# Kernel optimization log

Hardware: AMD Instinct MI355X
Metric: run time of the kernel (lower is better)

The kernel has to match this reference:

```python
import jax, jax.numpy as jnp
import numpy as np

B, CIN, HID, HEADS, K, STRIDE, PAD, W = 8, 256, 256, 8, 31, 1, 15, 16384
HD = HID // HEADS  # head dim
DN = ('NCHW', 'OIHW', 'NCHW')


def setup_inputs() -> dict:
    key = jax.random.key(0)
    ks = jax.random.split(key, 6)
    std = 1.0 / np.sqrt(HD)
    return dict(
        x=jax.random.normal(ks[0], (B, CIN, 1, W), jnp.float32),
        query=(jax.random.normal(ks[1], (HID,), jnp.float32) * std),
        Wk=(jax.random.normal(ks[2], (CIN, HID), jnp.float32) * std),
        Wk_bias=jnp.zeros((HID,), jnp.float32),
        rpe=0.02 * jax.random.normal(ks[3], (HEADS, 1, 1, K), jnp.float32),
        to_v_w=(jax.random.normal(ks[4], (HID, CIN, 1, 1), jnp.float32) / np.sqrt(CIN)),
        to_v_b=jnp.zeros((HID,), jnp.float32),
        to_out_w=(jax.random.normal(ks[5], (HID, HID, 1, 1), jnp.float32) / np.sqrt(HID)),
        to_out_b=jnp.zeros((HID,), jnp.float32),
    )


def reference(x, query, Wk, Wk_bias, rpe, to_v_w, to_v_b, to_out_w, to_out_b):
    Bsz = x.shape[0]
    # shared learned query -> [B, heads, hd], normalized and scaled
    q = jnp.broadcast_to(query, (Bsz, HID)).reshape(Bsz, HEADS, HD)
    q = q / (jnp.linalg.norm(q, axis=-1, keepdims=True) + 1e-6)
    q = q / np.sqrt(HD)
    # fused QK: (q @ Wk^T) @ x  -> cost [B, heads, 1, W]
    Wk_r = Wk.reshape(CIN, HEADS, HD)
    qWk = jnp.einsum('bhd,Dhd->bDh', q, Wk_r)          # [B, CIN, heads]
    cost = jnp.einsum('bDhw,bDc->bchw', x, qWk)        # [B, heads, 1, W]
    qWk_b = jnp.einsum('hd,bhd->bh', Wk_bias.reshape(HEADS, HD), q)
    cost = cost + qWk_b[:, :, None, None]
    cost_exp = jnp.exp(cost)
    # v = 1x1 conv (to_v)
    v = jnp.einsum('bdhw,od->bohw', x, to_v_w.reshape(HID, CIN)) + to_v_b[None, :, None, None]
    # exp-weighted values, grouped windowed sums
    vc = (cost_exp[:, :, None] * v.reshape(Bsz, HEADS, HD, 1, W)).reshape(Bsz, HID, 1, W)
    rpe_exp = jnp.exp(rpe)                             # [heads, 1, 1, K]
    kern_v = jnp.repeat(rpe_exp, HD, axis=0)           # [HID, 1, 1, K] depthwise
    sum_v = jax.lax.conv_general_dilated(
        vc, kern_v, (1, STRIDE), ((0, 0), (PAD, PAD)),
        feature_group_count=HID, dimension_numbers=DN)
    sum_c = jax.lax.conv_general_dilated(
        cost_exp, rpe_exp, (1, STRIDE), ((0, 0), (PAD, PAD)),
        feature_group_count=HEADS, dimension_numbers=DN)
    Wo = sum_v.shape[-1]
    out = sum_v.reshape(Bsz, HEADS, HD, 1, Wo) / sum_c.reshape(Bsz, HEADS, 1, 1, Wo)
    out = out.reshape(Bsz, HID, 1, Wo)
    # to_out 1x1 conv
    out = jnp.einsum('bdhw,od->bohw', out, to_out_w.reshape(HID, HID)) + to_out_b[None, :, None, None]
    return out
```

## Files before the change

### kernel.cpp

```cpp
#include <hip/hip_runtime.h>
#include <hip/hip_bf16.h>
#include <math.h>

#define BATCH  8
#define NHEADS 8
#define KW     31
#define W      16384

#define WS_QWKB 2048
#define WS_RPE  2056
#define OFF_WVH 9216
#define OFF_WOH (OFF_WVH + 131072)
#define OFF_CE  (OFF_WOH + 131072)

typedef __attribute__((ext_vector_type(8))) short  short8;
typedef __attribute__((ext_vector_type(4))) float  f32x4;

__device__ __forceinline__ float f4c(const float4& v, int i) {
  switch (i) { case 0: return v.x; case 1: return v.y; case 2: return v.z; default: return v.w; }
}
__device__ __forceinline__ unsigned short f2bf(float f) {
  union { __hip_bfloat16 h; unsigned short u; } cv; cv.h = __float2bfloat16(f); return cv.u;
}
__device__ __forceinline__ float bf2f(unsigned short u) {
  union { __hip_bfloat16 h; unsigned short u; } cv; cv.u = u; return __bfloat162float(cv.h);
}

__global__ __launch_bounds__(256) void prep_kernel(
    const float* __restrict__ query, const float* __restrict__ Wk,
    const float* __restrict__ Wkb, const float* __restrict__ rpe,
    const float* __restrict__ Wv, const float* __restrict__ Wo,
    float* __restrict__ ws, unsigned short* __restrict__ WvH,
    unsigned short* __restrict__ WoH) {
  int t = threadIdx.x, bid = blockIdx.x;
  if (bid == 0) {
    __shared__ float q_l[256];
    float qv = query[t];
    float ss = qv * qv;
    #pragma unroll
    for (int m = 16; m >= 1; m >>= 1) ss += __shfl_xor(ss, m, 32);
    qv = qv / (sqrtf(ss) + 1e-6f) * 0.17677669529663687f;
    q_l[t] = qv;
    __syncthreads();
    const float* wr = Wk + (size_t)t * 256;
    #pragma unroll
    for (int h = 0; h < 8; ++h) {
      float s = 0.f;
      #pragma unroll
      for (int d = 0; d < 32; ++d) s = fmaf(q_l[h*32 + d], wr[h*32 + d], s);
      ws[t*8 + h] = s;
    }
    float pb = Wkb[t] * q_l[t];
    #pragma unroll
    for (int m = 16; m >= 1; m >>= 1) pb += __shfl_xor(pb, m, 32);
    if ((t & 31) == 0) ws[WS_QWKB + (t >> 5)] = pb;
    if (t < NHEADS * KW) ws[WS_RPE + t] = __expf(rpe[t]);
  } else {
    const float* src = (bid <= 4) ? Wv : Wo;
    unsigned short* dst = (bid <= 4) ? WvH : WoH;
    int seg = (bid - 1) & 3;
    int base4 = seg * 4096;
    #pragma unroll
    for (int it = 0; it < 16; ++it) {
      int i4 = base4 + t + 256 * it;
      float4 v = ((const float4*)src)[i4];
      ushort4 o;
      o.x = f2bf(v.x); o.y = f2bf(v.y); o.z = f2bf(v.z); o.w = f2bf(v.w);
      ((ushort4*)dst)[i4] = o;
    }
  }
}

__global__ __launch_bounds__(256, 2) void xv_kernel(
    const float* __restrict__ x, const float* __restrict__ wsf,
    const unsigned short* __restrict__ A,
    const float* __restrict__ bias,
    float* __restrict__ ceout, float* __restrict__ vcout, int b0) {
  __shared__ float xs[64 * 260];
  __shared__ float cbuf[2048];
  __shared__ float ceL[512];
  __shared__ float biasL[256];

  int t = threadIdx.x;
  int bb = blockIdx.y, b = b0 + bb;
  int w0 = blockIdx.x * 64;
  biasL[t] = bias[t];

  {
    int rr = t >> 4, c2 = t & 15;
    #pragma unroll
    for (int db = 0; db < 4; ++db) {
      float4 v0 = *(const float4*)(x + ((size_t)b*256 + db*64 + rr*4 + 0)*W + w0 + c2*4);
      float4 v1 = *(const float4*)(x + ((size_t)b*256 + db*64 + rr*4 + 1)*W + w0 + c2*4);
      float4 v2 = *(const float4*)(x + ((size_t)b*256 + db*64 + rr*4 + 2)*W + w0 + c2*4);
      float4 v3 = *(const float4*)(x + ((size_t)b*256 + db*64 + rr*4 + 3)*W + w0 + c2*4);
      #pragma unroll
      for (int i = 0; i < 4; ++i) {
        float4 tv = make_float4(f4c(v0,i), f4c(v1,i), f4c(v2,i), f4c(v3,i));
        *(float4*)&xs[(c2*4 + i)*260 + db*64 + rr*4] = tv;
      }
    }
  }
  __syncthreads();

  int w = t & 63, q = t >> 6;
  int qu = __builtin_amdgcn_readfirstlane(q);

  f32x4 xr[16];
  {
    const float* xrow = &xs[w*260 + qu*64];
    #pragma unroll
    for (int i = 0; i < 16; ++i) xr[i] = *(const f32x4*)(xrow + 4*i);
    float ca[8] = {0,0,0,0,0,0,0,0};
    const float* qkb = wsf + (size_t)qu*64*8;
    #pragma unroll
    for (int k8 = 0; k8 < 8; ++k8) {
      const float* qr = qkb + 64*k8;
      #pragma unroll
      for (int e = 0; e < 4; ++e) {
        #pragma unroll
        for (int h = 0; h < 8; ++h) {
          ca[h] = fmaf(xr[2*k8][e],   qr[e*8 + h],     ca[h]);
          ca[h] = fmaf(xr[2*k8+1][e], qr[(e+4)*8 + h], ca[h]);
        }
      }
    }
    #pragma unroll
    for (int h = 0; h < 8; ++h) cbuf[t*8 + h] = ca[h];
  }
  __syncthreads();

  {
    unsigned short* hrow = (unsigned short*)xs + w*520 + qu*64;
    #pragma unroll
    for (int k8 = 0; k8 < 8; ++k8) {
      short8 hs, ls;
      #pragma unroll
      for (int e = 0; e < 4; ++e) {
        float a0 = xr[2*k8][e], a1 = xr[2*k8+1][e];
        unsigned short h0 = f2bf(a0), h1 = f2bf(a1);
        hs[e]   = (short)h0;  hs[e+4] = (short)h1;
        ls[e]   = (short)f2bf(a0 - bf2f(h0));
        ls[e+4] = (short)f2bf(a1 - bf2f(h1));
      }
      *(short8*)(hrow + 8*k8)       = hs;
      *(short8*)(hrow + 256 + 8*k8) = ls;
    }
  }
  __syncthreads();

  #pragma unroll
  for (int s = 0; s < 2; ++s) {
    int idx = t + 256*s;
    int h = idx >> 6, ww = idx & 63;
    float sum = cbuf[ww*8 + h] + cbuf[(64+ww)*8 + h] + cbuf[(128+ww)*8 + h]
              + cbuf[(192+ww)*8 + h] + wsf[WS_QWKB + h];
    float ce = __expf(sum);
    ceL[h*64 + ww] = ce;
    ceout[((size_t)bb*8 + h)*W + w0 + ww] = ce;
  }
  __syncthreads();

  int wid = t >> 6, quad = (t >> 4) & 3, m = t & 15;
  f32x4 acc[4][4];
  #pragma unroll
  for (int j = 0; j < 4; ++j)
    #pragma unroll
    for (int c = 0; c < 4; ++c) acc[j][c] = (f32x4){0.f, 0.f, 0.f, 0.f};

  const unsigned short* xsu = (const unsigned short*)xs;
  #pragma unroll
  for (int kk = 0; kk < 8; ++kk) {
    int ko = kk*32 + quad*8;
    short8 a[4], bh[4], bl[4];
    #pragma unroll
    for (int j = 0; j < 4; ++j)
      a[j] = *(const short8*)(A + (size_t)(64*wid + 16*j + m)*256 + ko);
    #pragma unroll
    for (int c = 0; c < 4; ++c) {
      int rw = 16*c + m;
      bh[c] = *(const short8*)(xsu + rw*520 + ko);
      bl[c] = *(const short8*)(xsu + rw*520 + 256 + ko);
    }
    #pragma unroll
    for (int j = 0; j < 4; ++j)
      #pragma unroll
      for (int c = 0; c < 4; ++c) {
        acc[j][c] = __builtin_amdgcn_mfma_f32_16x16x32_bf16(a[j], bh[c], acc[j][c], 0, 0, 0);
        acc[j][c] = __builtin_amdgcn_mfma_f32_16x16x32_bf16(a[j], bl[c], acc[j][c], 0, 0, 0);
      }
  }
  __syncthreads();

  #pragma unroll
  for (int j = 0; j < 4; ++j) {
    int ob = 64*wid + 16*j + 4*quad;
    int h = (64*wid + 16*j) >> 5;
    #pragma unroll
    for (int c = 0; c < 4; ++c) {
      int wc = 16*c + m;
      float ce = ceL[h*64 + wc];
      f32x4 r;
      #pragma unroll
      for (int i = 0; i < 4; ++i) r[i] = (acc[j][c][i] + biasL[ob + i]) * ce;
      *(f32x4*)(xs + wc*260 + ob) = r;
    }
  }
  __syncthreads();
  {
    size_t rowbase = (size_t)bb*W + w0;
    int w2 = t >> 2;
    #pragma unroll
    for (int k = 0; k < 16; ++k) {
      int oq = (t & 3)*64 + 4*k;
      f32x4 v = *(const f32x4*)(xs + w2*260 + oq);
      *(f32x4*)(vcout + (rowbase + w2)*256 + oq) = v;
    }
  }
}

template<int MODE>
__global__ __launch_bounds__(256, 2) void gemm_kernel(
    const unsigned short* __restrict__ A, const float* __restrict__ bias,
    const float* __restrict__ cost, unsigned short* Bact,
    float* outp, int b0) {
  __shared__ float smem[17408];
  __shared__ float ceL[512];
  __shared__ float biasL[256];
  unsigned short* smem_u = (unsigned short*)smem;

  int t = threadIdx.x;
  int bb = blockIdx.y;
  int w0 = blockIdx.x * 64;

  biasL[t] = bias[t];
  if (MODE == 0) {
    #pragma unroll
    for (int s = 0; s < 2; ++s) {
      int i = t + 256*s;
      ceL[i] = cost[((size_t)(bb*8 + (i >> 6)))*W + w0 + (i & 63)];
    }
  }
  {
    const unsigned short* src = Bact + ((size_t)bb*W + w0)*512;
    #pragma unroll
    for (int it = 0; it < 16; ++it) {
      int idx = t + 256*it;
      int r = idx >> 5, col = (idx & 31) * 8;
      short8 v = *(const short8*)(src + (size_t)idx*8);
      *(short8*)(smem_u + r*264 + col) = v;
    }
  }
  __syncthreads();

  int wid = t >> 6, quad = (t >> 4) & 3, m = t & 15;
  f32x4 acc[4][4];
  #pragma unroll
  for (int j = 0; j < 4; ++j)
    #pragma unroll
    for (int c = 0; c < 4; ++c) acc[j][c] = (f32x4){0.f, 0.f, 0.f, 0.f};

  #pragma unroll
  for (int kk = 0; kk < 8; ++kk) {
    int ko = kk*32 + quad*8;
    short8 a[4], bh[4], bl[4];
    #pragma unroll
    for (int j = 0; j < 4; ++j)
      a[j] = *(const short8*)(A + (size_t)(64*wid + 16*j + m)*256 + ko);
    #pragma unroll
    for (int c = 0; c < 4; ++c) {
      int row = 2*(16*c + m);
      bh[c] = *(const short8*)(smem_u + row*264 + ko);
      bl[c] = *(const short8*)(smem_u + (row+1)*264 + ko);
    }
    #pragma unroll
    for (int j = 0; j < 4; ++j)
      #pragma unroll
      for (int c = 0; c < 4; ++c) {
        acc[j][c] = __builtin_amdgcn_mfma_f32_16x16x32_bf16(a[j], bh[c], acc[j][c], 0, 0, 0);
        acc[j][c] = __builtin_amdgcn_mfma_f32_16x16x32_bf16(a[j], bl[c], acc[j][c], 0, 0, 0);
      }
  }
  __syncthreads();

  if (MODE == 0) {
    #pragma unroll
    for (int j = 0; j < 4; ++j) {
      int ob = 64*wid + 16*j + 4*quad;
      int h = (64*wid + 16*j) >> 5;
      #pragma unroll
      for (int c = 0; c < 4; ++c) {
        int w = 16*c + m;
        float ce = ceL[h*64 + w];
        f32x4 r;
        #pragma unroll
        for (int i = 0; i < 4; ++i) r[i] = (acc[j][c][i] + biasL[ob + i]) * ce;
        *(f32x4*)(smem + w*260 + ob) = r;
      }
    }
    __syncthreads();
    float* vcg = (float*)Bact;
    size_t rowbase = (size_t)bb*W + w0;
    int w = t >> 2;
    #pragma unroll
    for (int k = 0; k < 16; ++k) {
      int oq = (t & 3)*64 + 4*k;
      f32x4 v = *(const f32x4*)(smem + w*260 + oq);
      *(f32x4*)(vcg + (rowbase + w)*256 + oq) = v;
    }
  } else {
    #pragma unroll
    for (int j = 0; j < 4; ++j) {
      int ob = 64*wid + 16*j + 4*quad;
      #pragma unroll
      for (int c = 0; c < 4; ++c) {
        int w = 16*c + m;
        #pragma unroll
        for (int i = 0; i < 4; ++i) smem[(ob + i)*68 + w] = acc[j][c][i] + biasL[ob + i];
      }
    }
    __syncthreads();
    float* og = outp + (size_t)(b0 + bb)*256*W;
    #pragma unroll
    for (int i = 0; i < 4; ++i) {
      int o = (t >> 2) + 64*i;
      int c4 = t & 3;
      #pragma unroll
      for (int k = 0; k < 4; ++k) {
        int w = (c4 + 4*k)*4;
        f32x4 v = *(const f32x4*)(smem + o*68 + w);
        *(f32x4*)(og + (size_t)o*W + w0 + w) = v;
      }
    }
  }
}

__global__ __launch_bounds__(256, 2) void conv_kernel(
    const float* __restrict__ vc, const float* __restrict__ costexp,
    const float* __restrict__ rpe_ws, unsigned short* __restrict__ u) {
  __shared__ float vcl[94 * 132];
  __shared__ float cel[8 * 96];
  __shared__ float rcl[8 * 64];
  __shared__ float rpel[8 * 32];

  int t = threadIdx.x;
  int half = blockIdx.y, bb = blockIdx.z;
  int w0 = blockIdx.x * 64;

  rpel[t] = ((t & 31) < KW) ? rpe_ws[(t >> 5)*KW + (t & 31)] : 0.f;
  #pragma unroll
  for (int it = 0; it < 3; ++it) {
    int idx = t + 256*it;
    int h = idx / 96, c = idx % 96;
    if (h < 8) {
      int gw = w0 - 15 + c;
      cel[idx] = (c < 94 && gw >= 0 && gw < W) ? costexp[((size_t)bb*8 + h)*W + gw] : 0.f;
    }
  }
  #pragma unroll
  for (int it = 0; it < 12; ++it) {
    int idx = t + 256*it;
    int r = idx >> 5, c4 = (idx & 31)*4;
    if (r < 94) {
      int gw = w0 - 15 + r;
      float4 v = make_float4(0.f, 0.f, 0.f, 0.f);
      if (gw >= 0 && gw < W)
        v = *(const float4*)(vc + ((size_t)bb*W + gw)*256 + half*128 + c4);
      *(float4*)&vcl[r*132 + c4] = v;
    }
  }
  __syncthreads();

  #pragma unroll
  for (int s = 0; s < 2; ++s) {
    int idx = t + 256*s;
    int h = idx >> 6, w = idx & 63;
    float acc = 0.f;
    #pragma unroll
    for (int k = 0; k < KW; ++k) acc = fmaf(rpel[h*32 + k], cel[h*96 + w + k], acc);
    rcl[h*64 + w] = 1.0f / acc;
  }
  __syncthreads();

  int p = t & 63, g = t >> 6;
  int hh = half*4 + (p >> 4);
  float rp[KW];
  #pragma unroll
  for (int k = 0; k < KW; ++k) rp[k] = rpel[hh*32 + k];

  float ax[16], ay[16];
  #pragma unroll
  for (int i = 0; i < 16; ++i) { ax[i] = 0.f; ay[i] = 0.f; }
  #pragma unroll
  for (int s = 0; s < 46; ++s) {
    float2 v = *(const float2*)&vcl[(16*g + s)*132 + 2*p];
    #pragma unroll
    for (int i = 0; i < 16; ++i) {
      int k = s - i;
      if (k >= 0 && k < KW) {
        ax[i] = fmaf(rp[k], v.x, ax[i]);
        ay[i] = fmaf(rp[k], v.y, ay[i]);
      }
    }
  }
  #pragma unroll
  for (int i = 0; i < 16; ++i) {
    float rc = rcl[hh*64 + 16*g + i];
    float ux = ax[i] * rc, uy = ay[i] * rc;
    unsigned short hx = f2bf(ux), hy = f2bf(uy);
    unsigned short lx = f2bf(ux - bf2f(hx)), ly = f2bf(uy - bf2f(hy));
    unsigned short* ud = u + ((size_t)bb*W + w0 + 16*g + i)*512 + half*128 + 2*p;
    ushort2 hvv; hvv.x = hx; hvv.y = hy;
    ushort2 lvv; lvv.x = lx; lvv.y = ly;
    *(ushort2*)(ud)       = hvv;
    *(ushort2*)(ud + 256) = lvv;
  }
}

extern "C" void kernel_launch(void* const* d_in, const int* in_sizes, int n_in,
                              void* d_out, int out_size, void* d_ws, size_t ws_size,
                              hipStream_t stream) {
  const float* x     = (const float*)d_in[0];
  const float* query = (const float*)d_in[1];
  const float* Wk    = (const float*)d_in[2];
  const float* Wkb   = (const float*)d_in[3];
  const float* rpe   = (const float*)d_in[4];
  const float* Wv    = (const float*)d_in[5];
  const float* tvb   = (const float*)d_in[6];
  const float* Wo    = (const float*)d_in[7];
  const float* tob   = (const float*)d_in[8];
  float* out = (float*)d_out;
  char* wsb  = (char*)d_ws;
  float* wsf = (float*)d_ws;

  unsigned short* WvH = (unsigned short*)(wsb + OFF_WVH);
  unsigned short* WoH = (unsigned short*)(wsb + OFF_WOH);

  const size_t per_b = (size_t)8*W*4 + (size_t)W*256*4 + (size_t)W*512*2;
  int NB = (int)((ws_size > OFF_CE) ? ((ws_size - OFF_CE) / per_b) : 1);
  if (NB > BATCH) NB = BATCH;
  if (NB < 1) NB = 1;

  float*          ceB = (float*)(wsb + OFF_CE);
  float*          vcB = (float*)(wsb + OFF_CE + (size_t)NB*8*W*4);
  unsigned short* uB  = (unsigned short*)(wsb + OFF_CE + (size_t)NB*8*W*4 + (size_t)NB*W*256*4);

  prep_kernel<<<9, 256, 0, stream>>>(query, Wk, Wkb, rpe, Wv, Wo, wsf, WvH, WoH);

  for (int b0 = 0; b0 < BATCH; b0 += NB) {
    int nb = (BATCH - b0 < NB) ? (BATCH - b0) : NB;
    xv_kernel<<<dim3(256, nb), 256, 0, stream>>>(x, wsf, WvH, tvb, ceB, vcB, b0);
    conv_kernel<<<dim3(256, 2, nb), 256, 0, stream>>>(vcB, ceB, wsf + WS_RPE, uB);
    gemm_kernel<1><<<dim3(256, nb), 256, 0, stream>>>(WoH, tob, nullptr, uB, out, b0);
  }
}
```

Measured before the change: 470.0 us.

## Split work across more threads and blocks in xv, conv and out-GEMM kernels

xv_kernel moves to 512 threads per block, so each wave computes a 32-row slice of the value GEMM and half the K-reduction for the cost, with a two-phase cbuf reduction. conv_kernel splits channels into four quarters per block, which halves shared memory and per-thread accumulators. The output GEMM becomes a dedicated kernel that streams the hi and lo bf16 halves through a smaller LDS tile in two passes and writes results directly. The goal is higher occupancy and lower register and LDS pressure, at the cost of extra barriers, more redundant halo loads in conv, and uncoalesced strided output stores.

```diff
diff --git a/kernel.cpp b/kernel.cpp
--- a/kernel.cpp
+++ b/kernel.cpp
@@ -71,25 +71,27 @@
   }
 }
 
-__global__ __launch_bounds__(256, 2) void xv_kernel(
+__global__ __launch_bounds__(512, 4) void xv_kernel(
     const float* __restrict__ x, const float* __restrict__ wsf,
     const unsigned short* __restrict__ A,
     const float* __restrict__ bias,
     float* __restrict__ ceout, float* __restrict__ vcout, int b0) {
   __shared__ float xs[64 * 260];
-  __shared__ float cbuf[2048];
+  __shared__ float cbuf[4 * 576];
   __shared__ float ceL[512];
   __shared__ float biasL[256];
 
   int t = threadIdx.x;
   int bb = blockIdx.y, b = b0 + bb;
   int w0 = blockIdx.x * 64;
-  biasL[t] = bias[t];
+  if (t < 256) biasL[t] = bias[t];
 
   {
-    int rr = t >> 4, c2 = t & 15;
-    #pragma unroll
-    for (int db = 0; db < 4; ++db) {
+    int tt = t & 255, db2 = t >> 8;
+    int rr = tt >> 4, c2 = tt & 15;
+    #pragma unroll
+    for (int dd = 0; dd < 2; ++dd) {
+      int db = db2 * 2 + dd;
       float4 v0 = *(const float4*)(x + ((size_t)b*256 + db*64 + rr*4 + 0)*W + w0 + c2*4);
       float4 v1 = *(const float4*)(x + ((size_t)b*256 + db*64 + rr*4 + 1)*W + w0 + c2*4);
       float4 v2 = *(const float4*)(x + ((size_t)b*256 + db*64 + rr*4 + 2)*W + w0 + c2*4);
@@ -106,65 +108,80 @@
   int w = t & 63, q = t >> 6;
   int qu = __builtin_amdgcn_readfirstlane(q);
 
-  f32x4 xr[16];
+  f32x4 xr[8];
   {
-    const float* xrow = &xs[w*260 + qu*64];
-    #pragma unroll
-    for (int i = 0; i < 16; ++i) xr[i] = *(const f32x4*)(xrow + 4*i);
+    const float* xrow = &xs[w*260 + qu*32];
+    #pragma unroll
+    for (int i = 0; i < 8; ++i) xr[i] = *(const f32x4*)(xrow + 4*i);
     float ca[8] = {0,0,0,0,0,0,0,0};
-    const float* qkb = wsf + (size_t)qu*64*8;
-    #pragma unroll
-    for (int k8 = 0; k8 < 8; ++k8) {
-      const float* qr = qkb + 64*k8;
+    const float* qkb = wsf + (size_t)qu*256;
+    #pragma unroll
+    for (int k4 = 0; k4 < 8; ++k4) {
+      const float* qr = qkb + k4*32;
       #pragma unroll
       for (int e = 0; e < 4; ++e) {
         #pragma unroll
-        for (int h = 0; h < 8; ++h) {
-          ca[h] = fmaf(xr[2*k8][e],   qr[e*8 + h],     ca[h]);
-          ca[h] = fmaf(xr[2*k8+1][e], qr[(e+4)*8 + h], ca[h]);
+        for (int h = 0; h < 8; ++h)
+          ca[h] = fmaf(xr[k4][e], qr[e*8 + h], ca[h]);
+      }
+    }
+    if (q < 4) {
+      #pragma unroll
+      for (int h = 0; h < 8; ++h) cbuf[q*576 + w*9 + h] = ca[h];
+    } else {
+      #pragma unroll
+      for (int h = 0; h < 8; ++h) xr[h & 7][0] = xr[h & 7][0];
+      #pragma unroll
+      for (int h = 0; h < 8; ++h) {  asm volatile("" :: "v"(ca[h])); }
+    }
+    __syncthreads();
+
+    {
+      unsigned short* hrow = (unsigned short*)xs + w*520 + qu*32;
+      #pragma unroll
+      for (int kc = 0; kc < 4; ++kc) {
+        short8 hs, ls;
+        #pragma unroll
+        for (int e = 0; e < 4; ++e) {
+          float a0 = xr[2*kc][e], a1 = xr[2*kc+1][e];
+          unsigned short h0 = f2bf(a0), h1 = f2bf(a1);
+          hs[e]   = (short)h0;  hs[e+4] = (short)h1;
+          ls[e]   = (short)f2bf(a0 - bf2f(h0));
+          ls[e+4] = (short)f2bf(a1 - bf2f(h1));
         }
+        *(short8*)(hrow + 8*kc)       = hs;
+        *(short8*)(hrow + 256 + 8*kc) = ls;
       }
     }
-    #pragma unroll
-    for (int h = 0; h < 8; ++h) cbuf[t*8 + h] = ca[h];
-  }
-  __syncthreads();
-
-  {
-    unsigned short* hrow = (unsigned short*)xs + w*520 + qu*64;
-    #pragma unroll
-    for (int k8 = 0; k8 < 8; ++k8) {
-      short8 hs, ls;
-      #pragma unroll
-      for (int e = 0; e < 4; ++e) {
-        float a0 = xr[2*k8][e], a1 = xr[2*k8+1][e];
-        unsigned short h0 = f2bf(a0), h1 = f2bf(a1);
-        hs[e]   = (short)h0;  hs[e+4] = (short)h1;
-        ls[e]   = (short)f2bf(a0 - bf2f(h0));
-        ls[e+4] = (short)f2bf(a1 - bf2f(h1));
-      }
-      *(short8*)(hrow + 8*k8)       = hs;
-      *(short8*)(hrow + 256 + 8*k8) = ls;
-    }
-  }
-  __syncthreads();
-
-  #pragma unroll
-  for (int s = 0; s < 2; ++s) {
-    int idx = t + 256*s;
-    int h = idx >> 6, ww = idx & 63;
-    float sum = cbuf[ww*8 + h] + cbuf[(64+ww)*8 + h] + cbuf[(128+ww)*8 + h]
-              + cbuf[(192+ww)*8 + h] + wsf[WS_QWKB + h];
-    float ce = __expf(sum);
-    ceL[h*64 + ww] = ce;
-    ceout[((size_t)bb*8 + h)*W + w0 + ww] = ce;
+    float acc0;
+    {
+      int hR = t >> 6 & 7, wR = t & 63;
+      acc0 = cbuf[0*576 + wR*9 + hR] + cbuf[1*576 + wR*9 + hR]
+           + cbuf[2*576 + wR*9 + hR] + cbuf[3*576 + wR*9 + hR];
+    }
+    __syncthreads();
+    if (q >= 4) {
+      #pragma unroll
+      for (int h = 0; h < 8; ++h) cbuf[(q-4)*576 + w*9 + h] = ca[h];
+    }
+    __syncthreads();
+
+    {
+      int hR = t >> 6 & 7, wR = t & 63;
+      float sum = acc0 + cbuf[0*576 + wR*9 + hR] + cbuf[1*576 + wR*9 + hR]
+                + cbuf[2*576 + wR*9 + hR] + cbuf[3*576 + wR*9 + hR]
+                + wsf[WS_QWKB + hR];
+      float ce = __expf(sum);
+      ceL[hR*64 + wR] = ce;
+      ceout[((size_t)bb*8 + hR)*W + w0 + wR] = ce;
+    }
   }
   __syncthreads();
 
   int wid = t >> 6, quad = (t >> 4) & 3, m = t & 15;
-  f32x4 acc[4][4];
-  #pragma unroll
-  for (int j = 0; j < 4; ++j)
+  f32x4 acc[2][4];
+  #pragma unroll
+  for (int j = 0; j < 2; ++j)
     #pragma unroll
     for (int c = 0; c < 4; ++c) acc[j][c] = (f32x4){0.f, 0.f, 0.f, 0.f};
 
@@ -172,34 +189,28 @@
   #pragma unroll
   for (int kk = 0; kk < 8; ++kk) {
     int ko = kk*32 + quad*8;
-    short8 a[4], bh[4], bl[4];
-    #pragma unroll
-    for (int j = 0; j < 4; ++j)
-      a[j] = *(const short8*)(A + (size_t)(64*wid + 16*j + m)*256 + ko);
+    short8 a0 = *(const short8*)(A + (size_t)(32*wid + m)*256 + ko);
+    short8 a1 = *(const short8*)(A + (size_t)(32*wid + 16 + m)*256 + ko);
     #pragma unroll
     for (int c = 0; c < 4; ++c) {
       int rw = 16*c + m;
-      bh[c] = *(const short8*)(xsu + rw*520 + ko);
-      bl[c] = *(const short8*)(xsu + rw*520 + 256 + ko);
-    }
-    #pragma unroll
-    for (int j = 0; j < 4; ++j)
-      #pragma unroll
-      for (int c = 0; c < 4; ++c) {
-        acc[j][c] = __builtin_amdgcn_mfma_f32_16x16x32_bf16(a[j], bh[c], acc[j][c], 0, 0, 0);
-        acc[j][c] = __builtin_amdgcn_mfma_f32_16x16x32_bf16(a[j], bl[c], acc[j][c], 0, 0, 0);
-      }
-  }
-  __syncthreads();
-
-  #pragma unroll
-  for (int j = 0; j < 4; ++j) {
-    int ob = 64*wid + 16*j + 4*quad;
-    int h = (64*wid + 16*j) >> 5;
+      short8 bh = *(const short8*)(xsu + rw*520 + ko);
+      short8 bl = *(const short8*)(xsu + rw*520 + 256 + ko);
+      acc[0][c] = __builtin_amdgcn_mfma_f32_16x16x32_bf16(a0, bh, acc[0][c], 0, 0, 0);
+      acc[0][c] = __builtin_amdgcn_mfma_f32_16x16x32_bf16(a0, bl, acc[0][c], 0, 0, 0);
+      acc[1][c] = __builtin_amdgcn_mfma_f32_16x16x32_bf16(a1, bh, acc[1][c], 0, 0, 0);
+      acc[1][c] = __builtin_amdgcn_mfma_f32_16x16x32_bf16(a1, bl, acc[1][c], 0, 0, 0);
+    }
+  }
+  __syncthreads();
+
+  #pragma unroll
+  for (int j = 0; j < 2; ++j) {
+    int ob = 32*wid + 16*j + 4*quad;
     #pragma unroll
     for (int c = 0; c < 4; ++c) {
       int wc = 16*c + m;
-      float ce = ceL[h*64 + wc];
+      float ce = ceL[wid*64 + wc];
       f32x4 r;
       #pragma unroll
       for (int i = 0; i < 4; ++i) r[i] = (acc[j][c][i] + biasL[ob + i]) * ce;
@@ -208,194 +219,73 @@
   }
   __syncthreads();
   {
-    size_t rowbase = (size_t)bb*W + w0;
-    int w2 = t >> 2;
-    #pragma unroll
-    for (int k = 0; k < 16; ++k) {
-      int oq = (t & 3)*64 + 4*k;
-      f32x4 v = *(const f32x4*)(xs + w2*260 + oq);
-      *(f32x4*)(vcout + (rowbase + w2)*256 + oq) = v;
-    }
-  }
-}
-
-template<int MODE>
-__global__ __launch_bounds__(256, 2) void gemm_kernel(
-    const unsigned short* __restrict__ A, const float* __restrict__ bias,
-    const float* __restrict__ cost, unsigned short* Bact,
-    float* outp, int b0) {
-  __shared__ float smem[17408];
-  __shared__ float ceL[512];
-  __shared__ float biasL[256];
-  unsigned short* smem_u = (unsigned short*)smem;
-
-  int t = threadIdx.x;
-  int bb = blockIdx.y;
-  int w0 = blockIdx.x * 64;
-
-  biasL[t] = bias[t];
-  if (MODE == 0) {
-    #pragma unroll
-    for (int s = 0; s < 2; ++s) {
-      int i = t + 256*s;
-      ceL[i] = cost[((size_t)(bb*8 + (i >> 6)))*W + w0 + (i & 63)];
-    }
-  }
-  {
-    const unsigned short* src = Bact + ((size_t)bb*W + w0)*512;
-    #pragma unroll
-    for (int it = 0; it < 16; ++it) {
-      int idx = t + 256*it;
-      int r = idx >> 5, col = (idx & 31) * 8;
-      short8 v = *(const short8*)(src + (size_t)idx*8);
-      *(short8*)(smem_u + r*264 + col) = v;
-    }
-  }
-  __syncthreads();
-
-  int wid = t >> 6, quad = (t >> 4) & 3, m = t & 15;
-  f32x4 acc[4][4];
-  #pragma unroll
-  for (int j = 0; j < 4; ++j)
-    #pragma unroll
-    for (int c = 0; c < 4; ++c) acc[j][c] = (f32x4){0.f, 0.f, 0.f, 0.f};
-
-  #pragma unroll
-  for (int kk = 0; kk < 8; ++kk) {
-    int ko = kk*32 + quad*8;
-    short8 a[4], bh[4], bl[4];
-    #pragma unroll
-    for (int j = 0; j < 4; ++j)
-      a[j] = *(const short8*)(A + (size_t)(64*wid + 16*j + m)*256 + ko);
-    #pragma unroll
-    for (int c = 0; c < 4; ++c) {
-      int row = 2*(16*c + m);
-      bh[c] = *(const short8*)(smem_u + row*264 + ko);
-      bl[c] = *(const short8*)(smem_u + (row+1)*264 + ko);
-    }
-    #pragma unroll
-    for (int j = 0; j < 4; ++j)
-      #pragma unroll
-      for (int c = 0; c < 4; ++c) {
-        acc[j][c] = __builtin_amdgcn_mfma_f32_16x16x32_bf16(a[j], bh[c], acc[j][c], 0, 0, 0);
-        acc[j][c] = __builtin_amdgcn_mfma_f32_16x16x32_bf16(a[j], bl[c], acc[j][c], 0, 0, 0);
-      }
-  }
-  __syncthreads();
-
-  if (MODE == 0) {
-    #pragma unroll
-    for (int j = 0; j < 4; ++j) {
-      int ob = 64*wid + 16*j + 4*quad;
-      int h = (64*wid + 16*j) >> 5;
-      #pragma unroll
-      for (int c = 0; c < 4; ++c) {
-        int w = 16*c + m;
-        float ce = ceL[h*64 + w];
-        f32x4 r;
-        #pragma unroll
-        for (int i = 0; i < 4; ++i) r[i] = (acc[j][c][i] + biasL[ob + i]) * ce;
-        *(f32x4*)(smem + w*260 + ob) = r;
-      }
-    }
-    __syncthreads();
-    float* vcg = (float*)Bact;
-    size_t rowbase = (size_t)bb*W + w0;
-    int w = t >> 2;
-    #pragma unroll
-    for (int k = 0; k < 16; ++k) {
-      int oq = (t & 3)*64 + 4*k;
-      f32x4 v = *(const f32x4*)(smem + w*260 + oq);
-      *(f32x4*)(vcg + (rowbase + w)*256 + oq) = v;
-    }
-  } else {
-    #pragma unroll
-    for (int j = 0; j < 4; ++j) {
-      int ob = 64*wid + 16*j + 4*quad;
-      #pragma unroll
-      for (int c = 0; c < 4; ++c) {
-        int w = 16*c + m;
-        #pragma unroll
-        for (int i = 0; i < 4; ++i) smem[(ob + i)*68 + w] = acc[j][c][i] + biasL[ob + i];
-      }
-    }
-    __syncthreads();
-    float* og = outp + (size_t)(b0 + bb)*256*W;
-    #pragma unroll
-    for (int i = 0; i < 4; ++i) {
-      int o = (t >> 2) + 64*i;
-      int c4 = t & 3;
-      #pragma unroll
-      for (int k = 0; k < 4; ++k) {
-        int w = (c4 + 4*k)*4;
-        f32x4 v = *(const f32x4*)(smem + o*68 + w);
-        *(f32x4*)(og + (size_t)o*W + w0 + w) = v;
-      }
-    }
-  }
-}
-
-__global__ __launch_bounds__(256, 2) void conv_kernel(
+    float* vg = vcout + ((size_t)bb*W + w0)*256;
+    #pragma unroll
+    for (int it = 0; it < 8; ++it) {
+      int idx = t + 512*it;
+      int row = idx >> 6, c4 = (idx & 63)*4;
+      f32x4 v = *(const f32x4*)(xs + row*260 + c4);
+      *(f32x4*)(vg + (size_t)idx*4) = v;
+    }
+  }
+}
+
+__global__ __launch_bounds__(256, 4) void conv_kernel(
     const float* __restrict__ vc, const float* __restrict__ costexp,
     const float* __restrict__ rpe_ws, unsigned short* __restrict__ u) {
-  __shared__ float vcl[94 * 132];
-  __shared__ float cel[8 * 96];
-  __shared__ float rcl[8 * 64];
-  __shared__ float rpel[8 * 32];
+  __shared__ float vcl[94 * 68];
+  __shared__ float cel[2 * 96];
+  __shared__ float rcl[2 * 64];
+  __shared__ float rpel[2 * 32];
 
   int t = threadIdx.x;
-  int half = blockIdx.y, bb = blockIdx.z;
+  int qd = blockIdx.y, bb = blockIdx.z;
   int w0 = blockIdx.x * 64;
-
-  rpel[t] = ((t & 31) < KW) ? rpe_ws[(t >> 5)*KW + (t & 31)] : 0.f;
-  #pragma unroll
-  for (int it = 0; it < 3; ++it) {
+  int h0 = qd * 2;
+
+  if (t < 64) rpel[t] = ((t & 31) < KW) ? rpe_ws[(h0 + (t >> 5))*KW + (t & 31)] : 0.f;
+  if (t < 192) {
+    int h2 = t / 96, c = t % 96;
+    int gw = w0 - 15 + c;
+    cel[t] = (c < 94 && gw >= 0 && gw < W) ? costexp[((size_t)bb*8 + h0 + h2)*W + gw] : 0.f;
+  }
+  #pragma unroll
+  for (int it = 0; it < 6; ++it) {
     int idx = t + 256*it;
-    int h = idx / 96, c = idx % 96;
-    if (h < 8) {
-      int gw = w0 - 15 + c;
-      cel[idx] = (c < 94 && gw >= 0 && gw < W) ? costexp[((size_t)bb*8 + h)*W + gw] : 0.f;
-    }
-  }
-  #pragma unroll
-  for (int it = 0; it < 12; ++it) {
-    int idx = t + 256*it;
-    int r = idx >> 5, c4 = (idx & 31)*4;
+    int r = idx >> 4, c4 = (idx & 15)*4;
     if (r < 94) {
       int gw = w0 - 15 + r;
       float4 v = make_float4(0.f, 0.f, 0.f, 0.f);
       if (gw >= 0 && gw < W)
-        v = *(const float4*)(vc + ((size_t)bb*W + gw)*256 + half*128 + c4);
-      *(float4*)&vcl[r*132 + c4] = v;
-    }
-  }
-  __syncthreads();
-
-  #pragma unroll
-  for (int s = 0; s < 2; ++s) {
-    int idx = t + 256*s;
-    int h = idx >> 6, w = idx & 63;
+        v = *(const float4*)(vc + ((size_t)bb*W + gw)*256 + qd*64 + c4);
+      *(float4*)&vcl[r*68 + c4] = v;
+    }
+  }
+  __syncthreads();
+
+  if (t < 128) {
+    int h2 = t >> 6, w = t & 63;
     float acc = 0.f;
     #pragma unroll
-    for (int k = 0; k < KW; ++k) acc = fmaf(rpel[h*32 + k], cel[h*96 + w + k], acc);
-    rcl[h*64 + w] = 1.0f / acc;
-  }
-  __syncthreads();
-
-  int p = t & 63, g = t >> 6;
-  int hh = half*4 + (p >> 4);
+    for (int k = 0; k < KW; ++k) acc = fmaf(rpel[h2*32 + k], cel[h2*96 + w + k], acc);
+    rcl[h2*64 + w] = 1.0f / acc;
+  }
+  __syncthreads();
+
+  int p = t & 31, g = t >> 5;
+  int h2 = p >> 4;
   float rp[KW];
   #pragma unroll
-  for (int k = 0; k < KW; ++k) rp[k] = rpel[hh*32 + k];
-
-  float ax[16], ay[16];
-  #pragma unroll
-  for (int i = 0; i < 16; ++i) { ax[i] = 0.f; ay[i] = 0.f; }
-  #pragma unroll
-  for (int s = 0; s < 46; ++s) {
-    float2 v = *(const float2*)&vcl[(16*g + s)*132 + 2*p];
-    #pragma unroll
-    for (int i = 0; i < 16; ++i) {
+  for (int k = 0; k < KW; ++k) rp[k] = rpel[h2*32 + k];
+
+  float ax[8], ay[8];
+  #pragma unroll
+  for (int i = 0; i < 8; ++i) { ax[i] = 0.f; ay[i] = 0.f; }
+  #pragma unroll
+  for (int s = 0; s < 38; ++s) {
+    float2 v = *(const float2*)&vcl[(8*g + s)*68 + 2*p];
+    #pragma unroll
+    for (int i = 0; i < 8; ++i) {
       int k = s - i;
       if (k >= 0 && k < KW) {
         ax[i] = fmaf(rp[k], v.x, ax[i]);
@@ -404,16 +294,78 @@
     }
   }
   #pragma unroll
-  for (int i = 0; i < 16; ++i) {
-    float rc = rcl[hh*64 + 16*g + i];
+  for (int i = 0; i < 8; ++i) {
+    int o = 8*g + i;
+    float rc = rcl[h2*64 + o];
     float ux = ax[i] * rc, uy = ay[i] * rc;
     unsigned short hx = f2bf(ux), hy = f2bf(uy);
     unsigned short lx = f2bf(ux - bf2f(hx)), ly = f2bf(uy - bf2f(hy));
-    unsigned short* ud = u + ((size_t)bb*W + w0 + 16*g + i)*512 + half*128 + 2*p;
+    unsigned short* ud = u + ((size_t)bb*W + w0 + o)*512 + qd*64 + 2*p;
     ushort2 hvv; hvv.x = hx; hvv.y = hy;
     ushort2 lvv; lvv.x = lx; lvv.y = ly;
     *(ushort2*)(ud)       = hvv;
     *(ushort2*)(ud + 256) = lvv;
+  }
+}
+
+__global__ __launch_bounds__(256, 4) void gemm_out(
+    const unsigned short* __restrict__ A, const float* __restrict__ bias,
+    const unsigned short* __restrict__ u, float* __restrict__ outp, int b0) {
+  __shared__ unsigned short bs[64 * 264];
+  __shared__ float biasL[256];
+
+  int t = threadIdx.x;
+  int bb = blockIdx.y;
+  int w0 = blockIdx.x * 64;
+  biasL[t] = bias[t];
+
+  int wid = t >> 6, quad = (t >> 4) & 3, m = t & 15;
+  f32x4 acc[4][4];
+  #pragma unroll
+  for (int j = 0; j < 4; ++j)
+    #pragma unroll
+    for (int c = 0; c < 4; ++c) acc[j][c] = (f32x4){0.f, 0.f, 0.f, 0.f};
+
+  const unsigned short* src = u + ((size_t)bb*W + w0)*512;
+  #pragma unroll
+  for (int pass = 0; pass < 2; ++pass) {
+    #pragma unroll
+    for (int it = 0; it < 8; ++it) {
+      int idx = t + 256*it;
+      int row = idx >> 5, cc = (idx & 31)*8;
+      *(short8*)(bs + row*264 + cc) =
+          *(const short8*)(src + (size_t)row*512 + pass*256 + cc);
+    }
+    __syncthreads();
+    #pragma unroll
+    for (int kk = 0; kk < 8; ++kk) {
+      int ko = kk*32 + quad*8;
+      short8 a[4];
+      #pragma unroll
+      for (int j = 0; j < 4; ++j)
+        a[j] = *(const short8*)(A + (size_t)(64*wid + 16*j + m)*256 + ko);
+      #pragma unroll
+      for (int c = 0; c < 4; ++c) {
+        short8 bv = *(const short8*)(bs + (16*c + m)*264 + ko);
+        #pragma unroll
+        for (int j = 0; j < 4; ++j)
+          acc[j][c] = __builtin_amdgcn_mfma_f32_16x16x32_bf16(a[j], bv, acc[j][c], 0, 0, 0);
+      }
+    }
+    __syncthreads();
+  }
+
+  float* og = outp + (size_t)(b0 + bb)*256*W;
+  #pragma unroll
+  for (int j = 0; j < 4; ++j) {
+    int ob = 64*wid + 16*j + 4*quad;
+    #pragma unroll
+    for (int c = 0; c < 4; ++c) {
+      int w = w0 + 16*c + m;
+      #pragma unroll
+      for (int i = 0; i < 4; ++i)
+        og[(size_t)(ob + i)*W + w] = acc[j][c][i] + biasL[ob + i];
+    }
   }
 }
 
@@ -449,8 +401,8 @@
 
   for (int b0 = 0; b0 < BATCH; b0 += NB) {
     int nb = (BATCH - b0 < NB) ? (BATCH - b0) : NB;
-    xv_kernel<<<dim3(256, nb), 256, 0, stream>>>(x, wsf, WvH, tvb, ceB, vcB, b0);
-    conv_kernel<<<dim3(256, 2, nb), 256, 0, stream>>>(vcB, ceB, wsf + WS_RPE, uB);
-    gemm_kernel<1><<<dim3(256, nb), 256, 0, stream>>>(WoH, tob, nullptr, uB, out, b0);
-  }
-}
+    xv_kernel<<<dim3(256, nb), 512, 0, stream>>>(x, wsf, WvH, tvb, ceB, vcB, b0);
+    conv_kernel<<<dim3(256, 4, nb), 256, 0, stream>>>(vcB, ceB, wsf + WS_RPE, uB);
+    gemm_out<<<dim3(256, nb), 256, 0, stream>>>(WoH, tob, uB, out, b0);
+  }
+}
```

New measurement: 472.8 us. No clear change (+0.6%).
